# Optimization experiments

Measured on AMD Instinct MI355X. Metric: run time of the kernel, lower is better.

The kernel has to match this reference:

```python
import jax, jax.numpy as jnp
import numpy as np

D, H, COND, MLP_RATIO = 1024, 16, 1024, 4
HD = D // H
DFF = MLP_RATIO * D


def layer_norm(x, w, eps=1e-5):
    xf = x.astype(jnp.float32)
    mu = jnp.mean(xf, axis=-1, keepdims=True)
    var = jnp.mean((xf - mu) ** 2, axis=-1, keepdims=True)
    return (xf - mu) * jax.lax.rsqrt(var + eps) * w


def rms_norm(x, w, eps=1e-6):
    xf = x.astype(jnp.float32)
    rms = jnp.sqrt(jnp.mean(xf * xf, axis=-1, keepdims=True) + eps)
    return (xf / rms * w).astype(x.dtype)


def rotate_half(x):
    x1, x2 = x[..., : x.shape[-1] // 2], x[..., x.shape[-1] // 2:]
    return jnp.concatenate([-x2, x1], axis=-1)


def apply_rope(x, cos, sin):
    return x * cos + rotate_half(x) * sin


def setup_inputs() -> dict:
    key = jax.random.key(0)
    ks = jax.random.split(key, 16)
    B, S = 4, 2048
    pos = jnp.arange(S, dtype=jnp.float32)
    inv = 1.0 / (10000.0 ** (jnp.arange(0, HD, 2, dtype=jnp.float32) / HD))
    freqs = pos[:, None] * inv[None, :]              # (S, HD/2)
    emb = jnp.concatenate([freqs, freqs], axis=-1)   # (S, HD)
    return {
        "x": jax.random.normal(ks[0], (B, S, D), jnp.float32),
        "cos": jnp.cos(emb)[None, :, None, :],        # (1,S,1,HD)
        "sin": jnp.sin(emb)[None, :, None, :],
        "c": jax.random.normal(ks[1], (B, COND), jnp.float32),
        "norm1_w": jnp.ones((D,), jnp.float32),
        "Wqkv": jax.random.normal(ks[2], (D, 3 * D), jnp.float32) * 0.02,
        "Wout": jax.random.normal(ks[3], (D, D), jnp.float32) * 0.02,
        "q_norm_w": jnp.ones((HD,), jnp.float32),
        "k_norm_w": jnp.ones((HD,), jnp.float32),
        "norm2_w": jnp.ones((D,), jnp.float32),
        "W1": jax.random.normal(ks[4], (D, DFF), jnp.float32) * 0.02,
        "b1": jnp.zeros((DFF,), jnp.float32),
        "W2": jax.random.normal(ks[5], (DFF, D), jnp.float32) * 0.02,
        "b2": jnp.zeros((D,), jnp.float32),
        "ada_W": jax.random.normal(ks[6], (COND, 6 * D), jnp.float32) * 0.02,
        "ada_b": jnp.zeros((6 * D,), jnp.float32),
    }


def reference(x, cos, sin, c, norm1_w, Wqkv, Wout, q_norm_w, k_norm_w,
              norm2_w, W1, b1, W2, b2, ada_W, ada_b):
    B, S, _ = x.shape
    mod = (c @ ada_W + ada_b)[:, None, :]            # (B,1,6D)
    sh_msa, sc_msa, g_msa, sh_mlp, sc_mlp, g_mlp = jnp.split(mod, 6, axis=-1)

    x_norm = layer_norm(x, norm1_w) * (1 + sc_msa) + sh_msa
    qkv = (x_norm @ Wqkv).reshape(B, S, 3, H, HD)
    q, k, v = qkv[:, :, 0], qkv[:, :, 1], qkv[:, :, 2]  # (B,S,H,HD)
    q = apply_rope(rms_norm(q, q_norm_w), cos, sin)
    k = apply_rope(rms_norm(k, k_norm_w), cos, sin)

    scale = 1.0 / jnp.sqrt(jnp.float32(HD))
    logits = jnp.einsum('bqhd,bkhd->bhqk', q, k) * scale
    probs = jax.nn.softmax(logits, axis=-1)
    attn = jnp.einsum('bhqk,bkhd->bqhd', probs, v).reshape(B, S, D)

    x = x + g_msa * (attn @ Wout)

    x_norm = layer_norm(x, norm2_w) * (1 + sc_mlp) + sh_mlp
    h = jax.nn.gelu(x_norm @ W1 + b1, approximate=True)
    x = x + g_mlp * (h @ W2 + b2)
    return x
```

## Files before the change

### kernel.cpp

```cpp
#include <hip/hip_runtime.h>
#include <hip/hip_bf16.h>
#include <math.h>

typedef __bf16 bf16;
typedef __bf16 bf16x8 __attribute__((ext_vector_type(8)));
typedef __bf16 bf16x4 __attribute__((ext_vector_type(4)));
typedef float f32x4 __attribute__((ext_vector_type(4)));
typedef short s16x4 __attribute__((ext_vector_type(4)));

#define S_LEN 2048
#define NTOK 8192
#define DIM 1024
#define NH 16
#define HEADD 64
#define DFF 4096
#define MODD 6144

__device__ __forceinline__ float gelu_fast(float x) {
  float u = 0.7978845608028654f * (x + 0.044715f * x * x * x);
  float e = __builtin_amdgcn_exp2f(-2.8853900817779268f * u);
  return x * __builtin_amdgcn_rcpf(1.0f + e);
}

__device__ __forceinline__ void gl_lds16(const bf16* g, bf16* l) {
  __builtin_amdgcn_global_load_lds(
      (const __attribute__((address_space(1))) unsigned int*)g,
      (__attribute__((address_space(3))) unsigned int*)l, 16, 0, 0);
}

__global__ __launch_bounds__(256) void init_mod_kernel(
    const float* __restrict__ ada_b, float* __restrict__ mod) {
  int i = blockIdx.x * 256 + threadIdx.x;
  mod[i] = ada_b[i % MODD];
}

__global__ __launch_bounds__(256) void ada_gemm_kernel(
    const float* __restrict__ cnd, const float* __restrict__ W,
    float* __restrict__ mod) {
  int n = blockIdx.x * 256 + threadIdx.x;
  int k0 = blockIdx.y * 128;
  float a0 = 0.f, a1 = 0.f, a2 = 0.f, a3 = 0.f;
  for (int k = k0; k < k0 + 128; ++k) {
    float w = W[(size_t)k * MODD + n];
    a0 = fmaf(cnd[k], w, a0);
    a1 = fmaf(cnd[1024 + k], w, a1);
    a2 = fmaf(cnd[2048 + k], w, a2);
    a3 = fmaf(cnd[3072 + k], w, a3);
  }
  atomicAdd(&mod[n], a0);
  atomicAdd(&mod[MODD + n], a1);
  atomicAdd(&mod[2 * MODD + n], a2);
  atomicAdd(&mod[3 * MODD + n], a3);
}

__global__ __launch_bounds__(256) void transpose_cast_kernel(
    const float* __restrict__ W, bf16* __restrict__ Wt, int K, int N) {
  __shared__ float tile[32][33];
  int n0 = blockIdx.x * 32, k0 = blockIdx.y * 32;
  int r = threadIdx.x >> 3;
  int c4 = (threadIdx.x & 7) * 4;
  float4 v = *(const float4*)&W[(size_t)(k0 + r) * N + n0 + c4];
  tile[r][c4 + 0] = v.x; tile[r][c4 + 1] = v.y;
  tile[r][c4 + 2] = v.z; tile[r][c4 + 3] = v.w;
  __syncthreads();
  bf16x4 o;
  o[0] = (bf16)tile[c4 + 0][r];
  o[1] = (bf16)tile[c4 + 1][r];
  o[2] = (bf16)tile[c4 + 2][r];
  o[3] = (bf16)tile[c4 + 3][r];
  *(bf16x4*)&Wt[(size_t)(n0 + r) * K + k0 + c4] = o;
}

__global__ __launch_bounds__(256) void vtrans_kernel(
    const bf16* __restrict__ qkv, bf16* __restrict__ VT) {
  __shared__ __align__(16) bf16 t[64][72];
  const int bh = blockIdx.y;
  const int b = bh >> 4, h = bh & 15;
  const int s0 = blockIdx.x * 64;
  const int tid = threadIdx.x;
  {
    const int r = tid >> 2;
    const int c = (tid & 3) * 16;
    const bf16* src =
        qkv + (size_t)(b * S_LEN + s0 + r) * 3072 + 2048 + h * 64 + c;
    *(bf16x8*)&t[r][c] = *(const bf16x8*)src;
    *(bf16x8*)&t[r][c + 8] = *(const bf16x8*)(src + 8);
  }
  __syncthreads();
  {
    const int d = tid & 63;
    const int sc = (tid >> 6) * 16;
    bf16x8 o0, o1;
#pragma unroll
    for (int j = 0; j < 8; ++j) o0[j] = t[sc + j][d];
#pragma unroll
    for (int j = 0; j < 8; ++j) o1[j] = t[sc + 8 + j][d];
    bf16* dst = VT + (size_t)(bh * 64 + d) * S_LEN + s0 + sc;
    *(bf16x8*)dst = o0;
    *(bf16x8*)(dst + 8) = o1;
  }
}

__global__ __launch_bounds__(256) void ln_mod_kernel(
    const float* __restrict__ x, const float* __restrict__ w,
    const float* __restrict__ mod, int sh_off, int sc_off,
    bf16* __restrict__ out) {
  __shared__ float red[8];
  const int row = blockIdx.x;
  const int b = row >> 11;
  const int tid = threadIdx.x;
  const float4 v = ((const float4*)(x + (size_t)row * DIM))[tid];
  float s1 = v.x + v.y + v.z + v.w;
  float s2 = v.x * v.x + v.y * v.y + v.z * v.z + v.w * v.w;
  for (int off = 32; off > 0; off >>= 1) {
    s1 += __shfl_down(s1, off, 64);
    s2 += __shfl_down(s2, off, 64);
  }
  const int wid = tid >> 6;
  if ((tid & 63) == 0) { red[wid] = s1; red[4 + wid] = s2; }
  __syncthreads();
  s1 = red[0] + red[1] + red[2] + red[3];
  s2 = red[4] + red[5] + red[6] + red[7];
  const float mu = s1 * (1.0f / DIM);
  const float inv = rsqrtf(s2 * (1.0f / DIM) - mu * mu + 1e-5f);
  const int c = tid * 4;
  const float* mb = mod + (size_t)b * MODD;
  float xs[4] = {v.x, v.y, v.z, v.w};
  bf16x4 o;
#pragma unroll
  for (int j = 0; j < 4; ++j)
    o[j] = (bf16)(((xs[j] - mu) * inv) * w[c + j] * (1.0f + mb[sc_off + c + j]) +
                  mb[sh_off + c + j]);
  *(bf16x4*)(out + (size_t)row * DIM + c) = o;
}

template <int EPI, int MT, int BN>
__global__ __launch_bounds__(256) void gemm_bt(
    const bf16* __restrict__ A, const bf16* __restrict__ Bt,
    bf16* __restrict__ Cb, float* __restrict__ Cf,
    const float* __restrict__ bias, const float* __restrict__ gmod,
    const float* __restrict__ resid, const float* __restrict__ cosb,
    const float* __restrict__ sinb, const float* __restrict__ qw,
    const float* __restrict__ kw, int M, int N, int K) {
  constexpr int IM = MT / 32;
  constexpr int JN = BN / 32;
  constexpr int AG = MT / 64;
  constexpr int BG = BN / 64;
  __shared__ __align__(16) bf16 As[3][MT * 32];
  __shared__ __align__(16) bf16 Bs[3][BN * 32];
  const int tid = threadIdx.x;
  const int wid = tid >> 6;
  const int lane = tid & 63;
  const int l15 = lane & 15;
  const int quad = lane >> 4;

  const int gx = gridDim.x;
  const int flat = blockIdx.x + gx * blockIdx.y;
  const int xcd = flat & 7;
  const int idx = flat >> 3;
  const int ychunk = gridDim.y >> 3;
  const int bx = idx % gx;
  const int by = xcd * ychunk + idx / gx;
  const int m0 = by * MT;
  const int n0 = bx * BN;

  const int wm = (wid & 1) * (MT / 2);
  const int wn = (wid >> 1) * (BN / 2);

  const int srow = wid * 16 + (lane >> 2);
  const int scol = (lane & 3) * 8;
  const bf16* Ap = A + (size_t)(m0 + srow) * K + scol;
  const bf16* Bp = Bt + (size_t)(n0 + srow) * K + scol;

  auto stage = [&](int buf, int kt) {
#pragma unroll
    for (int g = 0; g < AG; ++g)
      gl_lds16(Ap + (size_t)g * 64 * K + kt, As[buf] + g * 2048 + wid * 512);
#pragma unroll
    for (int g = 0; g < BG; ++g)
      gl_lds16(Bp + (size_t)g * 64 * K + kt, Bs[buf] + g * 2048 + wid * 512);
  };

  stage(0, 0);
  stage(1, 32);

  f32x4 acc[IM][JN] = {};
  const int NT = K >> 5;
  int cur = 0, stg = 2;

  for (int t = 0; t < NT; ++t) {
    if (t + 2 < NT) {
      stage(stg, (t + 2) << 5);
      asm volatile("s_waitcnt vmcnt(8)" ::: "memory");
    } else if (t + 1 < NT) {
      asm volatile("s_waitcnt vmcnt(4)" ::: "memory");
    } else {
      asm volatile("s_waitcnt vmcnt(0)" ::: "memory");
    }
    __builtin_amdgcn_s_barrier();

    bf16x8 af[IM], bfr[JN];
#pragma unroll
    for (int i = 0; i < IM; ++i)
      af[i] = *(const bf16x8*)&As[cur][(wm + i * 16 + l15) * 32 + quad * 8];
#pragma unroll
    for (int j = 0; j < JN; ++j)
      bfr[j] = *(const bf16x8*)&Bs[cur][(wn + j * 16 + l15) * 32 + quad * 8];
    __builtin_amdgcn_s_setprio(1);
#pragma unroll
    for (int i = 0; i < IM; ++i)
#pragma unroll
      for (int j = 0; j < JN; ++j)
        acc[i][j] = __builtin_amdgcn_mfma_f32_16x16x32_bf16(af[i], bfr[j],
                                                            acc[i][j], 0, 0, 0);
    __builtin_amdgcn_s_setprio(0);
    __builtin_amdgcn_s_barrier();
    cur = (cur == 2) ? 0 : cur + 1;
    stg = (stg == 2) ? 0 : stg + 1;
  }

  if (EPI == 4 && n0 < 2048) {
    const float* nw = ((n0 + wn) < 1024) ? qw : kw;
    float wv[4];
#pragma unroll
    for (int j = 0; j < 4; ++j) wv[j] = nw[j * 16 + l15];
#pragma unroll
    for (int i = 0; i < IM; ++i) {
#pragma unroll
      for (int r = 0; r < 4; ++r) {
        const int m = m0 + wm + i * 16 + quad * 4 + r;
        const int s = m & (S_LEN - 1);
        float v[4];
        float ss = 0.f;
#pragma unroll
        for (int j = 0; j < 4; ++j) { v[j] = acc[i][j][r]; ss += v[j] * v[j]; }
        ss += __shfl_xor(ss, 1, 64);
        ss += __shfl_xor(ss, 2, 64);
        ss += __shfl_xor(ss, 4, 64);
        ss += __shfl_xor(ss, 8, 64);
        const float inv = rsqrtf(ss * (1.0f / HEADD) + 1e-6f);
        float xn[4];
#pragma unroll
        for (int j = 0; j < 4; ++j) xn[j] = v[j] * inv * wv[j];
#pragma unroll
        for (int j = 0; j < 4; ++j) {
          const int d = j * 16 + l15;
          const float rot = (j < 2) ? -xn[j + 2] : xn[j - 2];
          const float o = xn[j] * cosb[s * HEADD + d] + rot * sinb[s * HEADD + d];
          Cb[(size_t)m * N + n0 + wn + d] = (bf16)o;
        }
      }
    }
    return;
  }

#pragma unroll
  for (int i = 0; i < IM; ++i) {
#pragma unroll
    for (int r = 0; r < 4; ++r) {
      const int m = m0 + wm + i * 16 + quad * 4 + r;
#pragma unroll
      for (int j = 0; j < JN; ++j) {
        const int n = n0 + wn + j * 16 + l15;
        float v = acc[i][j][r];
        if (EPI == 0 || EPI == 4) {
          Cb[(size_t)m * N + n] = (bf16)v;
        } else if (EPI == 1) {
          const int b = m >> 11;
          Cf[(size_t)m * N + n] =
              resid[(size_t)m * N + n] + gmod[(size_t)b * MODD + n] * v;
        } else if (EPI == 2) {
          v += bias[n];
          Cb[(size_t)m * N + n] = (bf16)gelu_fast(v);
        } else {
          v += bias[n];
          const int b = m >> 11;
          Cf[(size_t)m * N + n] =
              resid[(size_t)m * N + n] + gmod[(size_t)b * MODD + n] * v;
        }
      }
    }
  }
}

__global__ __launch_bounds__(256) void attn_kernel(
    const bf16* __restrict__ qkv, const bf16* __restrict__ VT,
    bf16* __restrict__ Opart, float* __restrict__ psumbuf) {
  __shared__ __align__(16) bf16 Ks[4096];
  __shared__ __align__(16) bf16 Vs[4096];
  const int flat = blockIdx.x + 16 * (blockIdx.y + 64 * blockIdx.z);
  const int xcd = flat & 7;
  const int idx = flat >> 3;
  const int pair = xcd * 16 + (idx >> 4);
  const int qblk = idx & 15;
  const int bh = pair >> 1;
  const int split = pair & 1;
  const int b = bh >> 4;
  const int h = bh & 15;
  const int q0 = qblk * 128;
  const int tid = threadIdx.x;
  const int wid = tid >> 6;
  const int lane = tid & 63;
  const int l15 = lane & 15;
  const int quad = lane >> 4;

  bf16x8 aq[2][2];
#pragma unroll
  for (int i = 0; i < 2; ++i) {
    const int qrow = q0 + wid * 32 + i * 16 + l15;
    const size_t qbase = (size_t)(b * S_LEN + qrow) * (3 * DIM) + h * HEADD;
    aq[i][0] = *(const bf16x8*)(qkv + qbase + quad * 8);
    aq[i][1] = *(const bf16x8*)(qkv + qbase + 32 + quad * 8);
  }

  const int ksrow = (lane & 32) | ((lane & 4) << 2) | ((lane & 24) >> 1) | (lane & 3);
  const int ksw = ksrow & 7;
  const int vsw = lane & 7;
  const bf16* krow =
      qkv + (size_t)(b * S_LEN + split * 1024 + lane) * 3072 + DIM + h * HEADD;
  const bf16* vrow = VT + (size_t)(bh * 64 + lane) * S_LEN + split * 1024;

  bf16x8 kreg[2], vreg[2];
#pragma unroll
  for (int rr = 0; rr < 2; ++rr) {
    const int ck = wid + 4 * rr;
    kreg[rr] = *(const bf16x8*)(krow + ck * 8);
    vreg[rr] = *(const bf16x8*)(vrow + ck * 8);
  }

  const float cexp = 0.125f * 1.44269504f;
  const bf16 one = (bf16)1.0f;
  const bf16x8 ones8 = {one, one, one, one, one, one, one, one};
  f32x4 oacc[2][4] = {};
  f32x4 psacc[2] = {};

  for (int t = 0; t < 16; ++t) {
    __syncthreads();
#pragma unroll
    for (int rr = 0; rr < 2; ++rr) {
      const int ck = wid + 4 * rr;
      *(bf16x8*)&Ks[ksrow * 64 + ((ck ^ ksw) << 3)] = kreg[rr];
      *(bf16x8*)&Vs[lane * 64 + ((ck ^ vsw) << 3)] = vreg[rr];
    }
    __syncthreads();
    if (t < 15) {
      krow += 64 * 3072;
      vrow += 64;
#pragma unroll
      for (int rr = 0; rr < 2; ++rr) {
        const int ck = wid + 4 * rr;
        kreg[rr] = *(const bf16x8*)(krow + ck * 8);
        vreg[rr] = *(const bf16x8*)(vrow + ck * 8);
      }
    }

    f32x4 sc[2][4] = {};
    __builtin_amdgcn_s_setprio(1);
#pragma unroll
    for (int hh = 0; hh < 2; ++hh) {
#pragma unroll
      for (int cc = 0; cc < 4; ++cc) {
        const int row = cc * 16 + l15;
        const bf16x8 kf =
            *(const bf16x8*)&Ks[row * 64 + (((quad + 4 * hh) ^ (l15 & 7)) << 3)];
#pragma unroll
        for (int i = 0; i < 2; ++i)
          sc[i][cc] = __builtin_amdgcn_mfma_f32_16x16x32_bf16(kf, aq[i][hh],
                                                              sc[i][cc], 0, 0, 0);
      }
    }
    __builtin_amdgcn_s_setprio(0);

    bf16x8 pf[2][2];
#pragma unroll
    for (int i = 0; i < 2; ++i)
#pragma unroll
      for (int c2 = 0; c2 < 2; ++c2) {
        bf16x8 pb;
#pragma unroll
        for (int j = 0; j < 8; ++j) {
          const float p = __builtin_amdgcn_exp2f(
              fmaf(sc[i][2 * c2 + (j >> 2)][j & 3], cexp, -8.0f));
          pb[j] = (bf16)p;
        }
        pf[i][c2] = pb;
      }

    __builtin_amdgcn_s_setprio(1);
#pragma unroll
    for (int i = 0; i < 2; ++i)
#pragma unroll
      for (int c2 = 0; c2 < 2; ++c2)
        psacc[i] = __builtin_amdgcn_mfma_f32_16x16x32_bf16(pf[i][c2], ones8,
                                                           psacc[i], 0, 0, 0);
#pragma unroll
    for (int j = 0; j < 4; ++j) {
      const int d = 16 * j + l15;
      const int drow = d * 64;
      const int dsw = d & 7;
#pragma unroll
      for (int c2 = 0; c2 < 2; ++c2) {
        const bf16x8 vf =
            *(const bf16x8*)&Vs[drow + (((c2 * 4 + quad) ^ dsw) << 3)];
#pragma unroll
        for (int i = 0; i < 2; ++i)
          oacc[i][j] = __builtin_amdgcn_mfma_f32_16x16x32_bf16(pf[i][c2], vf,
                                                               oacc[i][j], 0, 0, 0);
      }
    }
    __builtin_amdgcn_s_setprio(0);
  }

#pragma unroll
  for (int i = 0; i < 2; ++i) {
    if (l15 == 0) {
#pragma unroll
      for (int r = 0; r < 4; ++r) {
        const int qrow = q0 + wid * 32 + i * 16 + quad * 4 + r;
        psumbuf[(size_t)split * (NTOK * NH) +
                (size_t)(b * S_LEN + qrow) * NH + h] = psacc[i][r];
      }
    }
#pragma unroll
    for (int r = 0; r < 4; ++r) {
      const int m = q0 + wid * 32 + i * 16 + quad * 4 + r;
#pragma unroll
      for (int j = 0; j < 4; ++j)
        Opart[(size_t)split * (NTOK * DIM) +
              ((size_t)(b * S_LEN + m) * NH + h) * HEADD + j * 16 + l15] =
            (bf16)oacc[i][j][r];
    }
  }
}

__global__ __launch_bounds__(256) void attn_reduce_kernel(
    const bf16* __restrict__ Opart, const float* __restrict__ psumbuf,
    bf16* __restrict__ attn) {
  const int g = blockIdx.x * 256 + threadIdx.x;
  const int token = g >> 7;
  const int rem = g & 127;
  const int h = rem >> 3;
  const int d0 = (rem & 7) * 8;
  const size_t off = ((size_t)token * NH + h) * HEADD + d0;
  const bf16x8 o0 = *(const bf16x8*)(Opart + off);
  const bf16x8 o1 = *(const bf16x8*)(Opart + (size_t)NTOK * DIM + off);
  const float l = psumbuf[token * NH + h] + psumbuf[NTOK * NH + token * NH + h];
  const float invl = 1.0f / l;
  bf16x8 o;
#pragma unroll
  for (int j = 0; j < 8; ++j)
    o[j] = (bf16)(((float)o0[j] + (float)o1[j]) * invl);
  *(bf16x8*)(attn + off) = o;
}

extern "C" void kernel_launch(void* const* d_in, const int* in_sizes, int n_in,
                              void* d_out, int out_size, void* d_ws,
                              size_t ws_size, hipStream_t stream) {
  const float* x = (const float*)d_in[0];
  const float* cosb = (const float*)d_in[1];
  const float* sinb = (const float*)d_in[2];
  const float* cnd = (const float*)d_in[3];
  const float* norm1_w = (const float*)d_in[4];
  const float* Wqkv = (const float*)d_in[5];
  const float* Wout = (const float*)d_in[6];
  const float* q_norm_w = (const float*)d_in[7];
  const float* k_norm_w = (const float*)d_in[8];
  const float* norm2_w = (const float*)d_in[9];
  const float* W1 = (const float*)d_in[10];
  const float* b1 = (const float*)d_in[11];
  const float* W2 = (const float*)d_in[12];
  const float* b2 = (const float*)d_in[13];
  const float* ada_W = (const float*)d_in[14];
  const float* ada_b = (const float*)d_in[15];
  float* out = (float*)d_out;

  char* p = (char*)d_ws;
  float* mod = (float*)p;   p += (size_t)4 * MODD * 4;
  bf16* WqkvT = (bf16*)p;   p += (size_t)3072 * 1024 * 2;
  bf16* WoutT = (bf16*)p;   p += (size_t)1024 * 1024 * 2;
  bf16* W1T = (bf16*)p;     p += (size_t)4096 * 1024 * 2;
  bf16* W2T = (bf16*)p;     p += (size_t)1024 * 4096 * 2;
  bf16* XN = (bf16*)p;      p += (size_t)NTOK * DIM * 2;
  bf16* QKV = (bf16*)p;     p += (size_t)NTOK * 3 * DIM * 2;
  bf16* ATTN = (bf16*)p;    p += (size_t)NTOK * DIM * 2;
  bf16* Hbuf = (bf16*)p;    p += (size_t)NTOK * DFF * 2;
  bf16* VT = Hbuf;
  bf16* Opart = Hbuf + (size_t)NTOK * DIM;
  float* psumbuf = (float*)(Hbuf + (size_t)3 * NTOK * DIM);

  init_mod_kernel<<<96, 256, 0, stream>>>(ada_b, mod);
  ada_gemm_kernel<<<dim3(24, 8), 256, 0, stream>>>(cnd, ada_W, mod);
  transpose_cast_kernel<<<dim3(96, 32), 256, 0, stream>>>(Wqkv, WqkvT, 1024, 3072);
  transpose_cast_kernel<<<dim3(32, 32), 256, 0, stream>>>(Wout, WoutT, 1024, 1024);
  transpose_cast_kernel<<<dim3(128, 32), 256, 0, stream>>>(W1, W1T, 1024, 4096);
  transpose_cast_kernel<<<dim3(32, 128), 256, 0, stream>>>(W2, W2T, 4096, 1024);
  ln_mod_kernel<<<NTOK, 256, 0, stream>>>(x, norm1_w, mod, 0, 1024, XN);
  gemm_bt<4, 128, 128><<<dim3(24, 64), 256, 0, stream>>>(
      XN, WqkvT, QKV, nullptr, nullptr, nullptr, nullptr, cosb, sinb,
      q_norm_w, k_norm_w, NTOK, 3072, 1024);
  vtrans_kernel<<<dim3(32, 64), 256, 0, stream>>>(QKV, VT);
  attn_kernel<<<dim3(16, 64, 2), 256, 0, stream>>>(QKV, VT, Opart, psumbuf);
  attn_reduce_kernel<<<4096, 256, 0, stream>>>(Opart, psumbuf, ATTN);
  gemm_bt<1, 128, 128><<<dim3(8, 64), 256, 0, stream>>>(
      ATTN, WoutT, nullptr, out, nullptr, mod + 2 * 1024, x, nullptr, nullptr,
      nullptr, nullptr, NTOK, 1024, 1024);
  ln_mod_kernel<<<NTOK, 256, 0, stream>>>(out, norm2_w, mod, 3 * 1024, 4 * 1024, XN);
  gemm_bt<2, 128, 128><<<dim3(32, 64), 256, 0, stream>>>(
      XN, W1T, Hbuf, nullptr, b1, nullptr, nullptr, nullptr, nullptr,
      nullptr, nullptr, NTOK, DFF, 1024);
  gemm_bt<3, 128, 128><<<dim3(8, 64), 256, 0, stream>>>(
      Hbuf, W2T, nullptr, out, b2, mod + 5 * 1024, out, nullptr, nullptr,
      nullptr, nullptr, NTOK, 1024, DFF);
  (void)in_sizes; (void)n_in; (void)out_size; (void)ws_size;
}
```

Baseline: 614.6 us.

## Drop split-K attention and reduce kernel; process 256 queries per block

Attention no longer splits the key range in two with a separate reduction pass. Each block now owns 256 query rows and walks all 2048 keys, normalising in-register before writing the final bf16 output. This removes the partial-output and row-sum round trip through memory and one kernel launch, and reuses each K/V tile across twice as many queries. The cost is fewer blocks (512 instead of 2048), longer serial loops and more accumulator registers per thread, which may lower occupancy.

Result: no change. 618.8 us (+0.7%).

```diff
diff --git a/kernel.cpp b/kernel.cpp
--- a/kernel.cpp
+++ b/kernel.cpp
@@ -285,29 +285,27 @@
 
 __global__ __launch_bounds__(256) void attn_kernel(
     const bf16* __restrict__ qkv, const bf16* __restrict__ VT,
-    bf16* __restrict__ Opart, float* __restrict__ psumbuf) {
+    bf16* __restrict__ attn) {
   __shared__ __align__(16) bf16 Ks[4096];
   __shared__ __align__(16) bf16 Vs[4096];
-  const int flat = blockIdx.x + 16 * (blockIdx.y + 64 * blockIdx.z);
+  const int flat = blockIdx.x + 8 * blockIdx.y;
   const int xcd = flat & 7;
   const int idx = flat >> 3;
-  const int pair = xcd * 16 + (idx >> 4);
-  const int qblk = idx & 15;
-  const int bh = pair >> 1;
-  const int split = pair & 1;
+  const int bh = xcd * 8 + (idx >> 3);
+  const int qblk = idx & 7;
   const int b = bh >> 4;
   const int h = bh & 15;
-  const int q0 = qblk * 128;
+  const int q0 = qblk * 256;
   const int tid = threadIdx.x;
   const int wid = tid >> 6;
   const int lane = tid & 63;
   const int l15 = lane & 15;
   const int quad = lane >> 4;
 
-  bf16x8 aq[2][2];
-#pragma unroll
-  for (int i = 0; i < 2; ++i) {
-    const int qrow = q0 + wid * 32 + i * 16 + l15;
+  bf16x8 aq[4][2];
+#pragma unroll
+  for (int i = 0; i < 4; ++i) {
+    const int qrow = q0 + wid * 64 + i * 16 + l15;
     const size_t qbase = (size_t)(b * S_LEN + qrow) * (3 * DIM) + h * HEADD;
     aq[i][0] = *(const bf16x8*)(qkv + qbase + quad * 8);
     aq[i][1] = *(const bf16x8*)(qkv + qbase + 32 + quad * 8);
@@ -317,8 +315,8 @@
   const int ksw = ksrow & 7;
   const int vsw = lane & 7;
   const bf16* krow =
-      qkv + (size_t)(b * S_LEN + split * 1024 + lane) * 3072 + DIM + h * HEADD;
-  const bf16* vrow = VT + (size_t)(bh * 64 + lane) * S_LEN + split * 1024;
+      qkv + (size_t)(b * S_LEN + lane) * 3072 + DIM + h * HEADD;
+  const bf16* vrow = VT + (size_t)(bh * 64 + lane) * S_LEN;
 
   bf16x8 kreg[2], vreg[2];
 #pragma unroll
@@ -331,10 +329,10 @@
   const float cexp = 0.125f * 1.44269504f;
   const bf16 one = (bf16)1.0f;
   const bf16x8 ones8 = {one, one, one, one, one, one, one, one};
-  f32x4 oacc[2][4] = {};
-  f32x4 psacc[2] = {};
-
-  for (int t = 0; t < 16; ++t) {
+  f32x4 oacc[4][4] = {};
+  f32x4 psacc[4] = {};
+
+  for (int t = 0; t < 32; ++t) {
     __syncthreads();
 #pragma unroll
     for (int rr = 0; rr < 2; ++rr) {
@@ -343,7 +341,7 @@
       *(bf16x8*)&Vs[lane * 64 + ((ck ^ vsw) << 3)] = vreg[rr];
     }
     __syncthreads();
-    if (t < 15) {
+    if (t < 31) {
       krow += 64 * 3072;
       vrow += 64;
 #pragma unroll
@@ -354,41 +352,43 @@
       }
     }
 
-    f32x4 sc[2][4] = {};
+    bf16x8 pf[4][2];
+#pragma unroll
+    for (int ip = 0; ip < 2; ++ip) {
+      f32x4 sc[2][4] = {};
+      __builtin_amdgcn_s_setprio(1);
+#pragma unroll
+      for (int hh = 0; hh < 2; ++hh) {
+#pragma unroll
+        for (int cc = 0; cc < 4; ++cc) {
+          const int row = cc * 16 + l15;
+          const bf16x8 kf =
+              *(const bf16x8*)&Ks[row * 64 + (((quad + 4 * hh) ^ (l15 & 7)) << 3)];
+#pragma unroll
+          for (int ii = 0; ii < 2; ++ii)
+            sc[ii][cc] = __builtin_amdgcn_mfma_f32_16x16x32_bf16(
+                kf, aq[2 * ip + ii][hh], sc[ii][cc], 0, 0, 0);
+        }
+      }
+      __builtin_amdgcn_s_setprio(0);
+#pragma unroll
+      for (int ii = 0; ii < 2; ++ii)
+#pragma unroll
+        for (int c2 = 0; c2 < 2; ++c2) {
+          bf16x8 pb;
+#pragma unroll
+          for (int j = 0; j < 8; ++j) {
+            const float p = __builtin_amdgcn_exp2f(
+                fmaf(sc[ii][2 * c2 + (j >> 2)][j & 3], cexp, -8.0f));
+            pb[j] = (bf16)p;
+          }
+          pf[2 * ip + ii][c2] = pb;
+        }
+    }
+
     __builtin_amdgcn_s_setprio(1);
 #pragma unroll
-    for (int hh = 0; hh < 2; ++hh) {
-#pragma unroll
-      for (int cc = 0; cc < 4; ++cc) {
-        const int row = cc * 16 + l15;
-        const bf16x8 kf =
-            *(const bf16x8*)&Ks[row * 64 + (((quad + 4 * hh) ^ (l15 & 7)) << 3)];
-#pragma unroll
-        for (int i = 0; i < 2; ++i)
-          sc[i][cc] = __builtin_amdgcn_mfma_f32_16x16x32_bf16(kf, aq[i][hh],
-                                                              sc[i][cc], 0, 0, 0);
-      }
-    }
-    __builtin_amdgcn_s_setprio(0);
-
-    bf16x8 pf[2][2];
-#pragma unroll
-    for (int i = 0; i < 2; ++i)
-#pragma unroll
-      for (int c2 = 0; c2 < 2; ++c2) {
-        bf16x8 pb;
-#pragma unroll
-        for (int j = 0; j < 8; ++j) {
-          const float p = __builtin_amdgcn_exp2f(
-              fmaf(sc[i][2 * c2 + (j >> 2)][j & 3], cexp, -8.0f));
-          pb[j] = (bf16)p;
-        }
-        pf[i][c2] = pb;
-      }
-
-    __builtin_amdgcn_s_setprio(1);
-#pragma unroll
-    for (int i = 0; i < 2; ++i)
+    for (int i = 0; i < 4; ++i)
 #pragma unroll
       for (int c2 = 0; c2 < 2; ++c2)
         psacc[i] = __builtin_amdgcn_mfma_f32_16x16x32_bf16(pf[i][c2], ones8,
@@ -403,7 +403,7 @@
         const bf16x8 vf =
             *(const bf16x8*)&Vs[drow + (((c2 * 4 + quad) ^ dsw) << 3)];
 #pragma unroll
-        for (int i = 0; i < 2; ++i)
+        for (int i = 0; i < 4; ++i)
           oacc[i][j] = __builtin_amdgcn_mfma_f32_16x16x32_bf16(pf[i][c2], vf,
                                                                oacc[i][j], 0, 0, 0);
       }
@@ -412,45 +412,17 @@
   }
 
 #pragma unroll
-  for (int i = 0; i < 2; ++i) {
-    if (l15 == 0) {
-#pragma unroll
-      for (int r = 0; r < 4; ++r) {
-        const int qrow = q0 + wid * 32 + i * 16 + quad * 4 + r;
-        psumbuf[(size_t)split * (NTOK * NH) +
-                (size_t)(b * S_LEN + qrow) * NH + h] = psacc[i][r];
-      }
-    }
+  for (int i = 0; i < 4; ++i) {
 #pragma unroll
     for (int r = 0; r < 4; ++r) {
-      const int m = q0 + wid * 32 + i * 16 + quad * 4 + r;
+      const int m = q0 + wid * 64 + i * 16 + quad * 4 + r;
+      const float invl = __builtin_amdgcn_rcpf(psacc[i][r]);
 #pragma unroll
       for (int j = 0; j < 4; ++j)
-        Opart[(size_t)split * (NTOK * DIM) +
-              ((size_t)(b * S_LEN + m) * NH + h) * HEADD + j * 16 + l15] =
-            (bf16)oacc[i][j][r];
-    }
-  }
-}
-
-__global__ __launch_bounds__(256) void attn_reduce_kernel(
-    const bf16* __restrict__ Opart, const float* __restrict__ psumbuf,
-    bf16* __restrict__ attn) {
-  const int g = blockIdx.x * 256 + threadIdx.x;
-  const int token = g >> 7;
-  const int rem = g & 127;
-  const int h = rem >> 3;
-  const int d0 = (rem & 7) * 8;
-  const size_t off = ((size_t)token * NH + h) * HEADD + d0;
-  const bf16x8 o0 = *(const bf16x8*)(Opart + off);
-  const bf16x8 o1 = *(const bf16x8*)(Opart + (size_t)NTOK * DIM + off);
-  const float l = psumbuf[token * NH + h] + psumbuf[NTOK * NH + token * NH + h];
-  const float invl = 1.0f / l;
-  bf16x8 o;
-#pragma unroll
-  for (int j = 0; j < 8; ++j)
-    o[j] = (bf16)(((float)o0[j] + (float)o1[j]) * invl);
-  *(bf16x8*)(attn + off) = o;
+        attn[((size_t)(b * S_LEN + m) * NH + h) * HEADD + j * 16 + l15] =
+            (bf16)(oacc[i][j][r] * invl);
+    }
+  }
 }
 
 extern "C" void kernel_launch(void* const* d_in, const int* in_sizes, int n_in,
@@ -485,8 +457,6 @@
   bf16* ATTN = (bf16*)p;    p += (size_t)NTOK * DIM * 2;
   bf16* Hbuf = (bf16*)p;    p += (size_t)NTOK * DFF * 2;
   bf16* VT = Hbuf;
-  bf16* Opart = Hbuf + (size_t)NTOK * DIM;
-  float* psumbuf = (float*)(Hbuf + (size_t)3 * NTOK * DIM);
 
   init_mod_kernel<<<96, 256, 0, stream>>>(ada_b, mod);
   ada_gemm_kernel<<<dim3(24, 8), 256, 0, stream>>>(cnd, ada_W, mod);
@@ -499,8 +469,7 @@
       XN, WqkvT, QKV, nullptr, nullptr, nullptr, nullptr, cosb, sinb,
       q_norm_w, k_norm_w, NTOK, 3072, 1024);
   vtrans_kernel<<<dim3(32, 64), 256, 0, stream>>>(QKV, VT);
-  attn_kernel<<<dim3(16, 64, 2), 256, 0, stream>>>(QKV, VT, Opart, psumbuf);
-  attn_reduce_kernel<<<4096, 256, 0, stream>>>(Opart, psumbuf, ATTN);
+  attn_kernel<<<dim3(8, 64), 256, 0, stream>>>(QKV, VT, ATTN);
   gemm_bt<1, 128, 128><<<dim3(8, 64), 256, 0, stream>>>(
       ATTN, WoutT, nullptr, out, nullptr, mod + 2 * 1024, x, nullptr, nullptr,
       nullptr, nullptr, NTOK, 1024, 1024);
```
